# Kernel tuning notes

Measured on AMD Instinct MI355X. Metric: run time of the kernel, lower is better.

Reference implementation:

```python
import jax, jax.numpy as jnp
import numpy as np
from jax import lax

B, D, S, H, W, T = 128, 512, 30, 14, 14, 12


def setup_inputs() -> dict:
    key = jax.random.key(0)
    ks = jax.random.split(key, 28)
    f = lambda k, shape: jax.random.normal(k, shape, jnp.float32) * 0.05
    return {
        "q": f(ks[0], (B, D)),
        "cws": f(ks[1], (B, D, S)),
        "KB": f(ks[2], (B, D, H, W)),
        "c0": f(ks[3], (B, D)),
        "m0": f(ks[4], (B, D)),
        "Wq": f(ks[5], (D, D)), "bq": f(ks[6], (D,)),
        "Wct": f(ks[7], (2 * D, D)), "bct": f(ks[8], (D,)),
        "wca": f(ks[9], (D,)), "bca": f(ks[10], ()),
        "Wm": f(ks[11], (D, D)), "bm": f(ks[12], (D,)),
        "Wkb": f(ks[13], (D, D)), "bkb": f(ks[14], (D,)),
        "Wrm": f(ks[15], (2 * D, D)), "brm": f(ks[16], (D,)),
        "wra": f(ks[17], (D,)), "bra": f(ks[18], ()),
        "Wwm": f(ks[19], (2 * D, D)), "bwm": f(ks[20], (D,)),
        "wwa": f(ks[21], (D,)), "bwa": f(ks[22], ()),
        "Wam": f(ks[23], (2 * D, D)), "bam": f(ks[24], (D,)),
        "Wg": f(ks[25], (D, D)), "bg": f(ks[26], (D,)),
        "steps": T,
    }


def _mac(q, cws, KB, c0, m0, Wq, bq, Wct, bct, wca, bca, Wm, bm, Wkb, bkb,
         Wrm, brm, wra, bra, Wwm, bwm, wwa, bwa, Wam, bam, Wg, bg, steps):
    b, d, h, w = KB.shape[0], KB.shape[1], KB.shape[2], KB.shape[3]
    KBp = jnp.transpose(KB, (0, 2, 3, 1))          # B,H,W,d
    KB2 = KBp @ Wkb + bkb                           # KB_transform (step-invariant)
    q_i = q @ Wq + bq                               # q_transform (step-invariant)

    nhist = steps + 1
    c_hist = jnp.zeros((nhist, b, d), KB.dtype).at[0].set(c0)
    m_hist = jnp.zeros((nhist, b, d), KB.dtype).at[0].set(m0)

    def step(carry, t):
        c_hist, m_hist, c_prev, m_prev = carry
        # ---- ControlUnit ----
        cq = jnp.concatenate([q_i, c_prev], axis=-1) @ Wct + bct   # B,d
        clog = jnp.einsum('bds,d->bs', cq[:, :, None] * cws, wca) + bca
        cattn = jax.nn.softmax(clog, axis=-1)                       # B,S
        c_i = jnp.einsum('bs,bds->bd', cattn, cws)
        # ---- ReadUnit ----
        mp = m_prev @ Wm + bm                                       # B,d
        I = mp[:, None, None, :] * KB2                              # B,H,W,d
        Im = jnp.concatenate([I, KBp], axis=-1) @ Wrm + brm         # B,H,W,d
        rlog = jnp.einsum('bhwd,d->bhw', c_i[:, None, None, :] * Im, wra) + bra
        rattn = jax.nn.softmax(rlog.reshape(b, -1), axis=-1).reshape(b, h, w)
        m_new = jnp.einsum('bhw,bhwd->bd', rattn, KBp)
        # ---- WriteUnit (self_attn + mem_gate) ----
        _m = jnp.concatenate([m_new, m_prev], axis=-1) @ Wwm + bwm
        slog = jnp.einsum('tbd,d->bt', c_i[None] * c_hist, wwa) + bwa
        valid = jnp.arange(nhist) <= t
        slog = jnp.where(valid[None, :], slog, jnp.float32(-1e9))
        sattn = jax.nn.softmax(slog, axis=-1)                       # B,T+1
        m_sa = jnp.einsum('bt,tbd->bd', sattn, m_hist)
        _m = jnp.concatenate([m_sa, _m], axis=-1) @ Wam + bam
        g = jax.nn.sigmoid(c_i @ Wg + bg)
        _m = g * m_prev + (1.0 - g) * _m
        c_hist = c_hist.at[t + 1].set(c_i)
        m_hist = m_hist.at[t + 1].set(_m)
        return (c_hist, m_hist, c_i, _m), None

    (c_hist, m_hist, c_last, m_last), _ = lax.scan(
        step, (c_hist, m_hist, c0, m0), jnp.arange(steps))
    return m_last


def reference(q, cws, KB, c0, m0, Wq, bq, Wct, bct, wca, bca, Wm, bm, Wkb, bkb,
              Wrm, brm, wra, bra, Wwm, bwm, wwa, bwa, Wam, bam, Wg, bg, steps):
    return _mac(q, cws, KB, c0, m0, Wq, bq, Wct, bct, wca, bca, Wm, bm, Wkb, bkb,
                Wrm, brm, wra, bra, Wwm, bwm, wwa, bwa, Wam, bam, Wg, bg, steps)
```

## Files before the change

### kernel.cpp

```cpp
#include <hip/hip_runtime.h>
#include <cstdint>

#define BB 128
#define DD 512
#define SS 30
#define PP 196
#define TT 12
#define BD (BB*DD)

typedef unsigned short ushortT;
typedef unsigned int uintT;

__device__ __forceinline__ float bf2f(ushortT u)
{
    return __uint_as_float(((uintT)u) << 16);
}
__device__ __forceinline__ ushortT f2bf(float f)
{
    uintT b = __float_as_uint(f);
    return (ushortT)((b + 0x7FFFu + ((b >> 16) & 1u)) >> 16);
}
__device__ __forceinline__ uintT pack2bf(float lo, float hi)
{
    return (uintT)f2bf(lo) | ((uintT)f2bf(hi) << 16);
}

struct GDesc {
    const float *A0, *A1;
    const ushortT *W0, *W1;
    const float *bias;
    float *out;
    const float *e1;
    int nparts, epi, mblk, nblk, aux;
};
struct GPack { GDesc d[6]; };

__global__ __launch_bounds__(256)
void gemm4(GPack pk)
{
    GDesc d = pk.d[blockIdx.z];
    if ((int)blockIdx.x >= d.mblk || (int)blockIdx.y >= d.nblk) return;
    const int tid  = threadIdx.x;
    const int lane = tid & 63;
    const int wv   = __builtin_amdgcn_readfirstlane(tid >> 6);

    if (d.epi == 5) {
        int bb = (blockIdx.x * 4 + blockIdx.y) * 2;
        #pragma unroll
        for (int b = bb; b < bb + 2; ++b) {
            const float* sat = d.e1 + b * 16;
            float a0 = 0.f, a1 = 0.f;
            for (int tp = 0; tp <= d.aux; ++tp) {
                float s = sat[tp];
                const float* mh = d.A0 + (size_t)tp * BD + (size_t)b * DD;
                a0 = fmaf(s, mh[tid], a0);
                a1 = fmaf(s, mh[tid + 256], a1);
            }
            d.out[(size_t)b * DD + tid] = a0;
            d.out[(size_t)b * DD + tid + 256] = a1;
        }
        return;
    }

    const int m0 = blockIdx.x * 8;
    const int c0 = blockIdx.y * 128;
    float accx[8], accy[8];
    #pragma unroll
    for (int m = 0; m < 8; ++m) { accx[m] = 0.f; accy[m] = 0.f; }

    for (int p = 0; p < d.nparts; ++p) {
        const float* A = p ? d.A1 : d.A0;
        const ushortT* W = p ? d.W1 : d.W0;
        const float* a = A + (size_t)m0 * 512 + wv * 128;
        const uintT* Wb = (const uintT*)(W + (size_t)(wv * 128) * 512 + c0) + lane;
        #pragma unroll 4
        for (int k = 0; k < 128; ++k) {
            uintT w = Wb[(size_t)k * 256];
            float wx = __uint_as_float(w << 16);
            float wy = __uint_as_float(w & 0xFFFF0000u);
            #pragma unroll
            for (int m = 0; m < 8; ++m) {
                float av = a[m * 512 + k];
                accx[m] = fmaf(av, wx, accx[m]);
                accy[m] = fmaf(av, wy, accy[m]);
            }
        }
    }

    __shared__ float red[4][8][128];
    #pragma unroll
    for (int m = 0; m < 8; ++m)
        *(float2*)&red[wv][m][lane * 2] = make_float2(accx[m], accy[m]);
    __syncthreads();

    for (int i = tid; i < 1024; i += 256) {
        int mm = i >> 7, cl = i & 127;
        float s = (red[0][mm][cl] + red[1][mm][cl])
                + (red[2][mm][cl] + red[3][mm][cl]);
        int row = m0 + mm, col = c0 + cl;
        size_t o = (size_t)row * 512 + col;
        if (d.epi == 0)      d.out[o] = s + d.bias[col];
        else if (d.epi == 1) { float v = s + d.bias[col];
                               d.out[o] = 1.f / (1.f + __expf(-v)); }
        else if (d.epi == 4) d.out[o] = s + d.e1[o];
        else if (d.epi == 7) ((ushortT*)d.out)[o] = f2bf(s);
        else                 d.out[o] = s;
    }
}

struct SP {
    const float *cq, *wca, *bca, *wra, *wwa, *bwa;
    const ushortT *cwsTh;
    float *c_hist, *sattn, *vb;
    const float *msa, *mnw, *gb, *b2;
    const ushortT *WamH, *WAH, *WBH;
    float *m_hist, *dst;
    int t;
};

__global__ __launch_bounds__(512)
void stepA(SP P)
{
    const int tid = threadIdx.x;
    const int lane = tid & 63;
    __shared__ float cqw[512], ciw[512];
    __shared__ float clog2[32], cattn[32], slog[16];
    __shared__ float red[8][2][128];

    if ((int)blockIdx.x < 128) {
        if (P.t >= TT) return;
        int b = blockIdx.x, w = tid >> 6, t = P.t;
        cqw[tid] = P.cq[(size_t)b*DD + tid] * P.wca[tid];
        __syncthreads();
        for (int s = w; s < SS; s += 8) {
            const ushortT* row = P.cwsTh + ((size_t)b*SS + s)*DD;
            float a = 0.f;
            #pragma unroll
            for (int j = 0; j < 8; ++j)
                a = fmaf(cqw[lane + 64*j], bf2f(row[lane + 64*j]), a);
            for (int off = 32; off; off >>= 1) a += __shfl_xor(a, off, 64);
            if (lane == 0) clog2[s] = a;
        }
        __syncthreads();
        if (tid < 32) {
            float v = (tid < SS) ? clog2[tid] + P.bca[0] : -1e30f;
            float mx = v;
            for (int off = 16; off; off >>= 1) mx = fmaxf(mx, __shfl_xor(mx, off, 32));
            float e = (tid < SS) ? __expf(v - mx) : 0.f;
            float sm = e;
            for (int off = 16; off; off >>= 1) sm += __shfl_xor(sm, off, 32);
            cattn[tid] = e / sm;
        }
        __syncthreads();
        {
            const ushortT* baseh = P.cwsTh + (size_t)b*SS*DD + tid;
            float acc = 0.f;
            #pragma unroll
            for (int j = 0; j < SS; ++j)
                acc = fmaf(cattn[j], bf2f(baseh[(size_t)j*DD]), acc);
            P.c_hist[(size_t)(t+1)*BD + (size_t)b*DD + tid] = acc;
            P.vb[(size_t)b*DD + tid] = acc * P.wra[tid];
            ciw[tid] = acc * P.wwa[tid];
        }
        __syncthreads();
        for (int tp = tid >> 6; tp <= t; tp += 8) {
            const float* ch = P.c_hist + (size_t)tp*BD + (size_t)b*DD;
            float a = 0.f;
            #pragma unroll
            for (int j = 0; j < 8; ++j)
                a = fmaf(ciw[lane + 64*j], ch[lane + 64*j], a);
            for (int off = 32; off; off >>= 1) a += __shfl_xor(a, off, 64);
            if (lane == 0) slog[tp] = a;
        }
        __syncthreads();
        if (tid < 16) {
            float v = (tid <= t) ? slog[tid] + P.bwa[0] : -1e30f;
            float mx = v;
            for (int off = 8; off; off >>= 1) mx = fmaxf(mx, __shfl_xor(mx, off, 16));
            float e = (tid <= t) ? __expf(v - mx) : 0.f;
            float sm = e;
            for (int off = 8; off; off >>= 1) sm += __shfl_xor(sm, off, 16);
            P.sattn[b*16 + tid] = e / sm;
        }
    } else {
        if (P.t == 0) return;
        int gb_ = blockIdx.x - 128;
        int mt = gb_ >> 2, nc = gb_ & 3;
        int wv = __builtin_amdgcn_readfirstlane(tid >> 6);
        const int koff = wv * 64;
        const float* mprev = P.m_hist + (size_t)(P.t - 1) * BD;
        const int r0 = mt * 2;
        float ax0 = 0.f, ay0 = 0.f, ax1 = 0.f, ay1 = 0.f;

        const float* As[3] = { P.msa, P.mnw, mprev };
        const ushortT* Ws[3] = { P.WamH, P.WAH, P.WBH };
        #pragma unroll
        for (int seg = 0; seg < 3; ++seg) {
            const float* a = As[seg] + (size_t)r0 * 512 + koff;
            const uintT* Wb = (const uintT*)(Ws[seg] + (size_t)koff * 512 + nc * 128) + lane;
            #pragma unroll 8
            for (int k = 0; k < 64; ++k) {
                uintT w = Wb[(size_t)k * 256];
                float wx = __uint_as_float(w << 16);
                float wy = __uint_as_float(w & 0xFFFF0000u);
                float av0 = a[k], av1 = a[512 + k];
                ax0 = fmaf(av0, wx, ax0); ay0 = fmaf(av0, wy, ay0);
                ax1 = fmaf(av1, wx, ax1); ay1 = fmaf(av1, wy, ay1);
            }
        }
        *(float2*)&red[wv][0][lane*2] = make_float2(ax0, ay0);
        *(float2*)&red[wv][1][lane*2] = make_float2(ax1, ay1);
        __syncthreads();
        if (tid < 256) {
            int mm = tid >> 7, cl = tid & 127;
            float s = 0.f;
            #pragma unroll
            for (int j = 0; j < 8; ++j) s += red[j][mm][cl];
            int row = r0 + mm, col = nc*128 + cl;
            size_t o = (size_t)row*512 + col;
            float v = s + P.b2[col];
            float g = P.gb[o];
            float pv = mprev[o];
            P.dst[o] = g*pv + (1.f - g)*v;
        }
    }
}

__global__ __launch_bounds__(256)
void read1y(const ushortT* __restrict__ KBh, const float* __restrict__ ubuf,
            const float* __restrict__ mp, const ushortT* __restrict__ WkbTh,
            const float* __restrict__ vW, float* __restrict__ rlogp)
{
    int b = blockIdx.x, dg = blockIdx.y, tid = threadIdx.x;
    int lane = tid & 63, w = tid >> 6;
    __shared__ float red[4][64];
    __shared__ float yb[64];
    {
        const float* ur = ubuf + (size_t)b*512;
        const float* mr = mp + (size_t)b*512;
        const ushortT* Wc = WkbTh + dg*64 + lane;
        float s = 0.f;
        for (int k = w*128; k < w*128 + 128; ++k)
            s = fmaf(ur[k]*mr[k], bf2f(Wc[(size_t)k*512]), s);
        red[w][lane] = s;
    }
    __syncthreads();
    if (tid < 64)
        yb[tid] = (red[0][tid]+red[1][tid]) + (red[2][tid]+red[3][tid])
                + vW[(size_t)b*512 + dg*64 + tid];
    __syncthreads();
    float a0=0.f, a1=0.f, a2=0.f, a3=0.f;
    if (tid < PP) {
        const ushortT* kb = KBh + ((size_t)b*512 + dg*64)*PP + tid;
        #pragma unroll 4
        for (int dd = 0; dd < 64; dd += 4) {
            a0 = fmaf(bf2f(kb[(size_t)(dd+0)*PP]), yb[dd+0], a0);
            a1 = fmaf(bf2f(kb[(size_t)(dd+1)*PP]), yb[dd+1], a1);
            a2 = fmaf(bf2f(kb[(size_t)(dd+2)*PP]), yb[dd+2], a2);
            a3 = fmaf(bf2f(kb[(size_t)(dd+3)*PP]), yb[dd+3], a3);
        }
    }
    rlogp[((size_t)b*8 + dg)*256 + tid] = (a0+a1)+(a2+a3);
}

__global__ __launch_bounds__(256)
void read2(const ushortT* __restrict__ KBh, const float* __restrict__ rlogp,
           float* __restrict__ m_new)
{
    int b = blockIdx.x, dg = blockIdx.y;
    int tid = threadIdx.x, lane = tid & 63, w = tid >> 6;
    __shared__ float ex[256];
    __shared__ float wred[4];

    float v = -1e30f;
    if (tid < PP) {
        const float* rp = rlogp + (size_t)b*2048 + tid;
        float t0 = rp[0]    + rp[256];
        float t1 = rp[512]  + rp[768];
        float t2 = rp[1024] + rp[1280];
        float t3 = rp[1536] + rp[1792];
        v = (t0+t1)+(t2+t3);
    }
    float mx = v;
    for (int off = 32; off; off >>= 1) mx = fmaxf(mx, __shfl_xor(mx, off, 64));
    if (lane == 0) wred[w] = mx;
    __syncthreads();
    float gmax = fmaxf(fmaxf(wred[0], wred[1]), fmaxf(wred[2], wred[3]));
    float e = (tid < PP) ? __expf(v - gmax) : 0.f;
    float sm = e;
    for (int off = 32; off; off >>= 1) sm += __shfl_xor(sm, off, 64);
    __syncthreads();
    if (lane == 0) wred[w] = sm;
    __syncthreads();
    float inv = 1.f / ((wred[0]+wred[1]) + (wred[2]+wred[3]));
    ex[tid] = e * inv;
    __syncthreads();

    #pragma unroll 2
    for (int i = 0; i < 16; ++i) {
        int d = dg*64 + w*16 + i;
        const ushortT* row = KBh + ((size_t)b*512 + d)*PP;
        float a = ex[lane]       * bf2f(row[lane])
                + ex[lane + 64]  * bf2f(row[lane + 64])
                + ex[lane + 128] * bf2f(row[lane + 128]);
        if (lane < PP - 192) a = fmaf(ex[lane + 192], bf2f(row[lane + 192]), a);
        for (int off = 32; off; off >>= 1) a += __shfl_xor(a, off, 64);
        if (lane == 0) m_new[(size_t)b*512 + d] = a;
    }
}

struct SetupP {
    const float *Wrm, *Wkb, *cws, *KB, *c0v, *m0v, *bwm;
    const float *Wam, *Wam_bot, *bam, *Wg, *Wm, *Wq, *Wct;
    float *c_hist, *m_hist, *b2;
    ushortT *KBh, *cwsTh, *WamH, *WgH, *WmH, *WqH, *WambH, *WctHt, *WctHb;
    ushortT *WrmTuH, *WrmTvH, *WkbTH;
};

__global__ __launch_bounds__(256)
void setup_misc(SetupP P)
{
    __shared__ float tile[32][33];
    int id = blockIdx.x, tid = threadIdx.x;

    if (id < 768) {
        int which = id >> 8, tj = id & 255;
        const float* src = (which == 0) ? P.Wrm
                         : (which == 1) ? (P.Wrm + 512*512) : P.Wkb;
        ushortT* dst = (which == 0) ? P.WrmTuH
                     : (which == 1) ? P.WrmTvH : P.WkbTH;
        int bx = (tj & 15) * 32, by = (tj >> 4) * 32;
        int tx = tid & 31, ty = tid >> 5;
        #pragma unroll
        for (int i = 0; i < 32; i += 8)
            tile[ty+i][tx] = src[(size_t)(by+ty+i)*512 + bx+tx];
        __syncthreads();
        #pragma unroll
        for (int i = 0; i < 32; i += 8)
            dst[(size_t)(bx+ty+i)*512 + by+tx] = f2bf(tile[tx][ty+i]);
    } else if (id < 2816) {
        int j = id - 768;
        int b = j >> 4, dc = j & 15;
        const float* src = P.cws + ((size_t)b*DD + dc*32) * SS;
        for (int i = tid; i < 1024; i += 256) {
            int r = i >> 5, s = i & 31;
            if (s < SS) tile[r][s] = src[(size_t)r*SS + s];
        }
        __syncthreads();
        for (int i = tid; i < 1024; i += 256) {
            int s = i >> 5, r = i & 31;
            if (s < SS)
                P.cwsTh[((size_t)b*SS + s)*DD + dc*32 + r] = f2bf(tile[r][s]);
        }
    } else if (id < 9088) {
        size_t i = ((size_t)(id - 2816) * 256 + tid) * 8;
        const float4* s4 = (const float4*)(P.KB + i);
        float4 v0 = s4[0], v1 = s4[1];
        uint4 o;
        o.x = pack2bf(v0.x, v0.y);
        o.y = pack2bf(v0.z, v0.w);
        o.z = pack2bf(v1.x, v1.y);
        o.w = pack2bf(v1.z, v1.w);
        *(uint4*)(P.KBh + i) = o;
    } else if (id < 9344) {
        int i = (id - 9088) * 256 + tid;
        P.c_hist[i] = P.c0v[i];
        P.m_hist[i] = P.m0v[i];
    } else if (id < 9352) {
        int lane = tid & 63, w = tid >> 6;
        int n = (id - 9344) * 64 + lane;
        float s = 0.f;
        for (int k = w*128; k < w*128 + 128; ++k)
            s = fmaf(P.bwm[k], P.Wam_bot[(size_t)k*512 + n], s);
        __shared__ float red[4][64];
        red[w][lane] = s;
        __syncthreads();
        if (tid < 64) {
            int nn = (id - 9344) * 64 + tid;
            P.b2[nn] = red[0][tid] + red[1][tid] + red[2][tid] + red[3][tid]
                     + P.bam[nn];
        }
    } else {
        int j = id - 9352;
        int which = j >> 7, blk = j & 127;
        const float* src = (which == 0) ? P.Wam
                         : (which == 1) ? P.Wg
                         : (which == 2) ? P.Wm
                         : (which == 3) ? P.Wq
                         : (which == 4) ? P.Wam_bot
                         : (which == 5) ? P.Wct : (P.Wct + 512*512);
        ushortT* dst = (which == 0) ? P.WamH
                     : (which == 1) ? P.WgH
                     : (which == 2) ? P.WmH
                     : (which == 3) ? P.WqH
                     : (which == 4) ? P.WambH
                     : (which == 5) ? P.WctHt : P.WctHb;
        size_t i = ((size_t)blk * 256 + tid) * 8;
        const float4* s4 = (const float4*)(src + i);
        float4 v0 = s4[0], v1 = s4[1];
        uint4 o;
        o.x = pack2bf(v0.x, v0.y);
        o.y = pack2bf(v0.z, v0.w);
        o.z = pack2bf(v1.x, v1.y);
        o.w = pack2bf(v1.z, v1.w);
        *(uint4*)(dst + i) = o;
    }
}

extern "C" void kernel_launch(void* const* d_in, const int* in_sizes, int n_in,
                              void* d_out, int out_size, void* d_ws, size_t ws_size,
                              hipStream_t stream)
{
    (void)in_sizes; (void)n_in; (void)out_size; (void)ws_size;
    const float* q   = (const float*)d_in[0];
    const float* cws = (const float*)d_in[1];
    const float* KB  = (const float*)d_in[2];
    const float* c0  = (const float*)d_in[3];
    const float* m0  = (const float*)d_in[4];
    const float* Wq  = (const float*)d_in[5];
    const float* bq  = (const float*)d_in[6];
    const float* Wct = (const float*)d_in[7];
    const float* bct = (const float*)d_in[8];
    const float* wca = (const float*)d_in[9];
    const float* bca = (const float*)d_in[10];
    const float* Wm  = (const float*)d_in[11];
    const float* bm  = (const float*)d_in[12];
    const float* Wkb = (const float*)d_in[13];
    const float* Wrm = (const float*)d_in[15];
    const float* wra = (const float*)d_in[17];
    const float* Wwm = (const float*)d_in[19];
    const float* bwm = (const float*)d_in[20];
    const float* wwa = (const float*)d_in[21];
    const float* bwa = (const float*)d_in[22];
    const float* Wam = (const float*)d_in[23];
    const float* bam = (const float*)d_in[24];
    const float* Wg  = (const float*)d_in[25];
    const float* bg  = (const float*)d_in[26];

    float* ws      = (float*)d_ws;
    float* c_hist  = ws;
    float* m_hist  = ws + 13*BD;
    float* qct     = ws + 26*BD;
    float* q_i     = ws + 27*BD;
    float* cq      = ws + 28*BD;
    float* mp      = ws + 29*BD;
    float* vb      = ws + 30*BD;
    float* ubuf    = ws + 31*BD;
    float* vW      = ws + 32*BD;
    float* gb      = ws + 33*BD;
    float* msa     = ws + 34*BD;
    float* mnw     = ws + 35*BD;
    float* sattn   = ws + 36*BD;
    float* rlogp   = ws + 37*BD;
    ushortT* WkbTH = (ushortT*)(ws + 49*BD);
    float* b2      = ws + 61*BD;
    ushortT* cwsTh = (ushortT*)(ws + 62*BD);
    ushortT* KBh   = (ushortT*)(ws + 92*BD);
    ushortT* WamH  = (ushortT*)(ws + 190*BD);
    ushortT* WAH   = (ushortT*)(ws + 192*BD);
    ushortT* WBH   = (ushortT*)(ws + 194*BD);
    ushortT* WgH   = (ushortT*)(ws + 196*BD);
    ushortT* WmH   = (ushortT*)(ws + 198*BD);
    ushortT* WqH   = (ushortT*)(ws + 200*BD);
    ushortT* WambH = (ushortT*)(ws + 202*BD);
    ushortT* WctHt = (ushortT*)(ws + 204*BD);
    ushortT* WctHb = (ushortT*)(ws + 206*BD);
    ushortT* WrmTuH= (ushortT*)(ws + 208*BD);
    ushortT* WrmTvH= (ushortT*)(ws + 210*BD);

    const float* Wam_bot = Wam + 512*512;
    const float* Wwm_bot = Wwm + 512*512;
    dim3 blk(256);
    GDesc Z = { nullptr,nullptr,nullptr,nullptr,nullptr,nullptr,nullptr,
                1, 6, 0, 0, 0 };

    {
        SetupP S;
        S.Wrm = Wrm; S.Wkb = Wkb; S.cws = cws; S.KB = KB;
        S.c0v = c0; S.m0v = m0; S.bwm = bwm;
        S.Wam = Wam; S.Wam_bot = Wam_bot; S.bam = bam;
        S.Wg = Wg; S.Wm = Wm; S.Wq = Wq; S.Wct = Wct;
        S.c_hist = c_hist; S.m_hist = m_hist; S.b2 = b2;
        S.KBh = KBh; S.cwsTh = cwsTh;
        S.WamH = WamH; S.WgH = WgH; S.WmH = WmH; S.WqH = WqH;
        S.WambH = WambH; S.WctHt = WctHt; S.WctHb = WctHb;
        S.WrmTuH = WrmTuH; S.WrmTvH = WrmTvH; S.WkbTH = WkbTH;
        setup_misc<<<dim3(10248), blk, 0, stream>>>(S);
    }
    {
        GPack pk;
        pk.d[0] = { Wwm, nullptr, WambH, nullptr, nullptr, (float*)WAH,
                    nullptr, 1, 7, 64, 4, 0 };
        pk.d[1] = { Wwm_bot, nullptr, WambH, nullptr, nullptr, (float*)WBH,
                    nullptr, 1, 7, 64, 4, 0 };
        pk.d[2] = { q, nullptr, WqH, nullptr, bq, q_i, nullptr,
                    1, 0, 16, 4, 0 };
        pk.d[3] = Z; pk.d[4] = Z; pk.d[5] = Z;
        gemm4<<<dim3(64,4,3), blk, 0, stream>>>(pk);
    }
    {
        GPack pk;
        pk.d[0] = { q_i, nullptr, WctHt, nullptr, bct, qct, nullptr,
                    1, 0, 16, 4, 0 };
        pk.d[1] = { q_i, c0, WctHt, WctHb, bct, cq, nullptr,
                    2, 0, 16, 4, 0 };
        pk.d[2] = Z; pk.d[3] = Z; pk.d[4] = Z; pk.d[5] = Z;
        gemm4<<<dim3(16,4,2), blk, 0, stream>>>(pk);
    }

    for (int t = 0; t <= TT; ++t) {
        {
            SP P;
            P.cq = cq; P.cwsTh = cwsTh;
            P.wca = wca; P.bca = bca; P.wra = wra; P.wwa = wwa; P.bwa = bwa;
            P.c_hist = c_hist; P.sattn = sattn; P.vb = vb;
            P.msa = msa; P.mnw = mnw; P.gb = gb; P.b2 = b2;
            P.WamH = WamH; P.WAH = WAH; P.WBH = WBH;
            P.m_hist = m_hist;
            P.dst = (t == TT) ? (float*)d_out : (m_hist + (size_t)t * BD);
            P.t = t;
            stepA<<<dim3(384), dim3(512), 0, stream>>>(P);
        }
        if (t == TT) break;

        float* c_i = c_hist + (size_t)(t+1) * BD;
        {
            GPack pk;
            pk.d[0] = { vb, nullptr, WrmTuH, nullptr, nullptr, ubuf, nullptr,
                        1, 6, 16, 4, 0 };
            pk.d[1] = { vb, nullptr, WrmTvH, nullptr, nullptr, vW, nullptr,
                        1, 6, 16, 4, 0 };
            pk.d[2] = { c_i, nullptr, WgH, nullptr, bg, gb, nullptr,
                        1, 1, 16, 4, 0 };
            pk.d[3] = { c_i, nullptr, WctHb, nullptr, nullptr, cq, qct,
                        1, 4, 16, 4, 0 };
            pk.d[4] = { m_hist + (size_t)t * BD, nullptr, WmH, nullptr, bm, mp,
                        nullptr, 1, 0, 16, 4, 0 };
            pk.d[5] = { m_hist, nullptr, nullptr, nullptr, nullptr, msa, sattn,
                        1, 5, 16, 4, t };
            gemm4<<<dim3(16,4,6), blk, 0, stream>>>(pk);
        }
        read1y<<<dim3(BB,8), blk, 0, stream>>>(KBh, ubuf, mp, WkbTH, vW, rlogp);
        read2<<<dim3(BB,8), blk, 0, stream>>>(KBh, rlogp, mnw);
    }
}
```

Baseline: 747.8 us.

## Fuse read-attention softmax and KB weighted sum into stepA GEMM blocks

Removes the separate read2 kernel and computes the read softmax and the attention-weighted KB sum inside the stepA memory-update blocks, keeping m_new in shared memory instead of global. This saves one launch per step and a global write/read of m_new. In exchange, each of the four column-chunk blocks redundantly recomputes the KB reduction for its two rows. The KB reads also become strided per lane rather than coalesced.

```diff
diff --git a/kernel.cpp b/kernel.cpp
--- a/kernel.cpp
+++ b/kernel.cpp
@@ -112,7 +112,9 @@
     const float *cq, *wca, *bca, *wra, *wwa, *bwa;
     const ushortT *cwsTh;
     float *c_hist, *sattn, *vb;
-    const float *msa, *mnw, *gb, *b2;
+    const float *msa, *gb, *b2;
+    const float *rlogp;
+    const ushortT *KBh;
     const ushortT *WamH, *WAH, *WBH;
     float *m_hist, *dst;
     int t;
@@ -126,6 +128,9 @@
     __shared__ float cqw[512], ciw[512];
     __shared__ float clog2[32], cattn[32], slog[16];
     __shared__ float red[8][2][128];
+    __shared__ float exsh[2][200];
+    __shared__ float mnwsh[2][512];
+    __shared__ float wred[4];
 
     if ((int)blockIdx.x < 128) {
         if (P.t >= TT) return;
@@ -190,14 +195,80 @@
         const int koff = wv * 64;
         const float* mprev = P.m_hist + (size_t)(P.t - 1) * BD;
         const int r0 = mt * 2;
+
+        #pragma unroll
+        for (int bb = 0; bb < 2; ++bb) {
+            float v = -1e30f;
+            if (tid < PP) {
+                const float* rp = P.rlogp + (size_t)(r0 + bb)*2048 + tid;
+                float t0 = rp[0]    + rp[256];
+                float t1 = rp[512]  + rp[768];
+                float t2 = rp[1024] + rp[1280];
+                float t3 = rp[1536] + rp[1792];
+                v = (t0+t1)+(t2+t3);
+            }
+            float mx = v;
+            for (int off = 32; off; off >>= 1) mx = fmaxf(mx, __shfl_xor(mx, off, 64));
+            if (lane == 0 && wv < 4) wred[wv] = mx;
+            __syncthreads();
+            float gmax = fmaxf(fmaxf(wred[0], wred[1]), fmaxf(wred[2], wred[3]));
+            float e = (tid < PP) ? __expf(v - gmax) : 0.f;
+            float sm = e;
+            for (int off = 32; off; off >>= 1) sm += __shfl_xor(sm, off, 64);
+            __syncthreads();
+            if (lane == 0 && wv < 4) wred[wv] = sm;
+            __syncthreads();
+            float inv = 1.f / ((wred[0]+wred[1]) + (wred[2]+wred[3]));
+            if (tid < PP) exsh[bb][tid] = e * inv;
+            __syncthreads();
+        }
+
+        {
+            int dd = koff + lane;
+            const ushortT* kb0 = P.KBh + ((size_t)(r0+0)*512 + dd)*PP;
+            const ushortT* kb1 = P.KBh + ((size_t)(r0+1)*512 + dd)*PP;
+            float a0 = 0.f, a1 = 0.f, c0v = 0.f, c1v = 0.f;
+            #pragma unroll 4
+            for (int p = 0; p < PP; p += 2) {
+                a0  = fmaf(exsh[0][p],   bf2f(kb0[p]),   a0);
+                a1  = fmaf(exsh[0][p+1], bf2f(kb0[p+1]), a1);
+                c0v = fmaf(exsh[1][p],   bf2f(kb1[p]),   c0v);
+                c1v = fmaf(exsh[1][p+1], bf2f(kb1[p+1]), c1v);
+            }
+            mnwsh[0][dd] = a0 + a1;
+            mnwsh[1][dd] = c0v + c1v;
+        }
+        __syncthreads();
+
         float ax0 = 0.f, ay0 = 0.f, ax1 = 0.f, ay1 = 0.f;
-
-        const float* As[3] = { P.msa, P.mnw, mprev };
-        const ushortT* Ws[3] = { P.WamH, P.WAH, P.WBH };
-        #pragma unroll
-        for (int seg = 0; seg < 3; ++seg) {
-            const float* a = As[seg] + (size_t)r0 * 512 + koff;
-            const uintT* Wb = (const uintT*)(Ws[seg] + (size_t)koff * 512 + nc * 128) + lane;
+        {
+            const float* a = P.msa + (size_t)r0 * 512 + koff;
+            const uintT* Wb = (const uintT*)(P.WamH + (size_t)koff * 512 + nc * 128) + lane;
+            #pragma unroll 8
+            for (int k = 0; k < 64; ++k) {
+                uintT w = Wb[(size_t)k * 256];
+                float wx = __uint_as_float(w << 16);
+                float wy = __uint_as_float(w & 0xFFFF0000u);
+                float av0 = a[k], av1 = a[512 + k];
+                ax0 = fmaf(av0, wx, ax0); ay0 = fmaf(av0, wy, ay0);
+                ax1 = fmaf(av1, wx, ax1); ay1 = fmaf(av1, wy, ay1);
+            }
+        }
+        {
+            const uintT* Wb = (const uintT*)(P.WAH + (size_t)koff * 512 + nc * 128) + lane;
+            #pragma unroll 8
+            for (int k = 0; k < 64; ++k) {
+                uintT w = Wb[(size_t)k * 256];
+                float wx = __uint_as_float(w << 16);
+                float wy = __uint_as_float(w & 0xFFFF0000u);
+                float av0 = mnwsh[0][koff + k], av1 = mnwsh[1][koff + k];
+                ax0 = fmaf(av0, wx, ax0); ay0 = fmaf(av0, wy, ay0);
+                ax1 = fmaf(av1, wx, ax1); ay1 = fmaf(av1, wy, ay1);
+            }
+        }
+        {
+            const float* a = mprev + (size_t)r0 * 512 + koff;
+            const uintT* Wb = (const uintT*)(P.WBH + (size_t)koff * 512 + nc * 128) + lane;
             #pragma unroll 8
             for (int k = 0; k < 64; ++k) {
                 uintT w = Wb[(size_t)k * 256];
@@ -261,52 +332,6 @@
         }
     }
     rlogp[((size_t)b*8 + dg)*256 + tid] = (a0+a1)+(a2+a3);
-}
-
-__global__ __launch_bounds__(256)
-void read2(const ushortT* __restrict__ KBh, const float* __restrict__ rlogp,
-           float* __restrict__ m_new)
-{
-    int b = blockIdx.x, dg = blockIdx.y;
-    int tid = threadIdx.x, lane = tid & 63, w = tid >> 6;
-    __shared__ float ex[256];
-    __shared__ float wred[4];
-
-    float v = -1e30f;
-    if (tid < PP) {
-        const float* rp = rlogp + (size_t)b*2048 + tid;
-        float t0 = rp[0]    + rp[256];
-        float t1 = rp[512]  + rp[768];
-        float t2 = rp[1024] + rp[1280];
-        float t3 = rp[1536] + rp[1792];
-        v = (t0+t1)+(t2+t3);
-    }
-    float mx = v;
-    for (int off = 32; off; off >>= 1) mx = fmaxf(mx, __shfl_xor(mx, off, 64));
-    if (lane == 0) wred[w] = mx;
-    __syncthreads();
-    float gmax = fmaxf(fmaxf(wred[0], wred[1]), fmaxf(wred[2], wred[3]));
-    float e = (tid < PP) ? __expf(v - gmax) : 0.f;
-    float sm = e;
-    for (int off = 32; off; off >>= 1) sm += __shfl_xor(sm, off, 64);
-    __syncthreads();
-    if (lane == 0) wred[w] = sm;
-    __syncthreads();
-    float inv = 1.f / ((wred[0]+wred[1]) + (wred[2]+wred[3]));
-    ex[tid] = e * inv;
-    __syncthreads();
-
-    #pragma unroll 2
-    for (int i = 0; i < 16; ++i) {
-        int d = dg*64 + w*16 + i;
-        const ushortT* row = KBh + ((size_t)b*512 + d)*PP;
-        float a = ex[lane]       * bf2f(row[lane])
-                + ex[lane + 64]  * bf2f(row[lane + 64])
-                + ex[lane + 128] * bf2f(row[lane + 128]);
-        if (lane < PP - 192) a = fmaf(ex[lane + 192], bf2f(row[lane + 192]), a);
-        for (int off = 32; off; off >>= 1) a += __shfl_xor(a, off, 64);
-        if (lane == 0) m_new[(size_t)b*512 + d] = a;
-    }
 }
 
 struct SetupP {
@@ -449,7 +474,6 @@
     float* vW      = ws + 32*BD;
     float* gb      = ws + 33*BD;
     float* msa     = ws + 34*BD;
-    float* mnw     = ws + 35*BD;
     float* sattn   = ws + 36*BD;
     float* rlogp   = ws + 37*BD;
     ushortT* WkbTH = (ushortT*)(ws + 49*BD);
@@ -514,7 +538,8 @@
             P.cq = cq; P.cwsTh = cwsTh;
             P.wca = wca; P.bca = bca; P.wra = wra; P.wwa = wwa; P.bwa = bwa;
             P.c_hist = c_hist; P.sattn = sattn; P.vb = vb;
-            P.msa = msa; P.mnw = mnw; P.gb = gb; P.b2 = b2;
+            P.msa = msa; P.gb = gb; P.b2 = b2;
+            P.rlogp = rlogp; P.KBh = KBh;
             P.WamH = WamH; P.WAH = WAH; P.WBH = WBH;
             P.m_hist = m_hist;
             P.dst = (t == TT) ? (float*)d_out : (m_hist + (size_t)t * BD);
@@ -541,6 +566,5 @@
             gemm4<<<dim3(16,4,6), blk, 0, stream>>>(pk);
         }
         read1y<<<dim3(BB,8), blk, 0, stream>>>(KBh, ubuf, mp, WkbTH, vW, rlogp);
-        read2<<<dim3(BB,8), blk, 0, stream>>>(KBh, rlogp, mnw);
-    }
-}
+    }
+}
```

Result: slower. 1.932 ms (+158.4%).
